# Optimization experiments

Hardware: AMD Instinct MI355X
Metric: run time of the kernel (lower is better)

## Reference

```python
import jax, jax.numpy as jnp
import numpy as np

NEG = -1e30  # log-space 'zero' (avoid actual -inf for stable grads)
BLANK = 1


def _ctc_single(logp, target, il, tl):
    # logp: [T, V] log-probabilities; target: [S] int; il, tl: scalar lengths
    T, V = logp.shape
    S = target.shape[0]
    L = 2 * S + 1
    # extended label sequence: blank, t0, blank, t1, ..., blank
    ext = jnp.full((L,), BLANK, dtype=target.dtype).at[1::2].set(target)
    prev2 = jnp.concatenate([jnp.full((2,), -1, dtype=ext.dtype), ext[:-2]])
    can_skip = (ext != BLANK) & (ext != prev2)  # allowed s-2 transition
    valid = jnp.arange(L) < (2 * tl + 1)  # mask lattice positions beyond target length
    lp_ext = logp[:, ext]  # [T, L] gather of emission log-probs along the lattice

    alpha0 = jnp.full((L,), NEG, dtype=logp.dtype)
    alpha0 = alpha0.at[0].set(lp_ext[0, 0]).at[1].set(lp_ext[0, 1])
    alpha0 = jnp.where(valid, alpha0, NEG)

    def step(alpha, inp):
        t, lp = inp  # lp: [L]
        a1 = jnp.concatenate([jnp.full((1,), NEG, alpha.dtype), alpha[:-1]])
        a2 = jnp.concatenate([jnp.full((2,), NEG, alpha.dtype), alpha[:-2]])
        a2 = jnp.where(can_skip, a2, NEG)
        new = jnp.logaddexp(jnp.logaddexp(alpha, a1), a2) + lp
        new = jnp.where(valid, new, NEG)
        new = jnp.where(t < il, new, alpha)  # freeze alpha past input length
        return new, None

    alpha, _ = jax.lax.scan(step, alpha0, (jnp.arange(1, T), lp_ext[1:]))
    end = 2 * tl
    ll = jnp.logaddexp(alpha[end], alpha[end - 1])
    loss = -ll
    # zero_infinity=True: clamp non-finite / degenerate losses to 0
    loss = jnp.where(loss < 1e29, loss, 0.0)
    return loss


def setup_inputs() -> dict:
    key = jax.random.key(0)
    k1, k2, k3, k4 = jax.random.split(key, 4)
    B, T, V, S = 64, 2000, 256, 400
    # module expects log-probabilities over phonemes
    log_probs = jax.nn.log_softmax(
        jax.random.normal(k1, (B, T, V), dtype=jnp.float32), axis=-1)
    # targets avoid blank_id=1 (labels in [2, V))
    targets = jax.random.randint(k2, (B, S), 2, V, dtype=jnp.int32)
    input_lengths = jax.random.randint(k3, (B,), T // 2, T + 1, dtype=jnp.int32)
    target_lengths = jax.random.randint(k4, (B,), S // 2, S + 1, dtype=jnp.int32)
    return {"log_probs": log_probs, "targets": targets,
            "input_lengths": input_lengths, "target_lengths": target_lengths}


def reference(log_probs, targets, input_lengths, target_lengths):
    losses = jax.vmap(_ctc_single)(log_probs, targets, input_lengths, target_lengths)
    # nn.CTCLoss reduction='mean': per-sample loss divided by target length, then batch mean
    return jnp.mean(losses / target_lengths.astype(losses.dtype))
```

## Files before the change

kernel.cpp:

```cpp
#include <hip/hip_runtime.h>

#define LOG2E 1.4426950408889634f
#define LN2   0.6931471805599453f

namespace {
constexpr int B    = 64;
constexpr int T    = 2000;
constexpr int V    = 256;
constexpr int S    = 400;
constexpr int CHK  = 8;
constexpr int NCTP = 250;
constexpr int BSTR = 20;
constexpr int KP   = 408;
constexpr size_t GELEM  = (size_t)B * NCTP * KP * 8;
constexpr size_t GBYTES = GELEM * 2;
constexpr size_t LAOFF  = GBYTES / 4;
constexpr size_t LGOFF  = LAOFF + 64 * 1024;
constexpr size_t REQBYTES = GBYTES + 2 * 64 * 1024 * 4;
constexpr int LSTR = 260;
constexpr int NW7  = 7;
constexpr int NCT7 = 250;
constexpr int BST7 = 12;
}

using h8 = __attribute__((ext_vector_type(8))) _Float16;

__device__ __forceinline__ float fexp2(float x){ return __builtin_amdgcn_exp2f(x); }
__device__ __forceinline__ float flog2(float x){ return __builtin_amdgcn_logf(x); }

__device__ __forceinline__ float wave_shr1(float x) {
  int v = __builtin_amdgcn_update_dpp(0, __builtin_bit_cast(int, x),
                                      0x138, 0xf, 0xf, true);
  return __builtin_bit_cast(float, v);
}
__device__ __forceinline__ int wave_shr1_i(int x) {
  return __builtin_amdgcn_update_dpp(0, x, 0x138, 0xf, 0xf, true);
}
__device__ __forceinline__ float wave_shl1(float x) {
  int v = __builtin_amdgcn_update_dpp(0, __builtin_bit_cast(int, x),
                                      0x130, 0xf, 0xf, true);
  return __builtin_bit_cast(float, v);
}
__device__ __forceinline__ int wave_shl1_i(int x) {
  return __builtin_amdgcn_update_dpp(0, x, 0x130, 0xf, 0xf, true);
}

__global__ __launch_bounds__(512)
void ctc_gather_kernel(const float* __restrict__ logp,
                       const int* __restrict__ targets,
                       _Float16* __restrict__ G)
{
  const int tile = blockIdx.x;
  const int b    = blockIdx.y;
  const int tid  = threadIdx.x;
  const int i0   = tile * 64;
  const float* lp = logp + (size_t)b * T * V;
  const int*   tg = targets + (size_t)b * S;

  __shared__ float ls[64 * LSTR];
  __shared__ int   tgs[S];

  for (int f = tid; f < 64 * 64; f += 512) {
    const int row = f >> 6, c4 = f & 63;
    int t = i0 + 1 + row; if (t > T - 1) t = T - 1;
    float4 v = ((const float4*)(lp + (size_t)t * V))[c4];
    *(float4*)&ls[row * LSTR + c4 * 4] = v;
  }
  for (int k = tid; k < S; k += 512) tgs[k] = tg[k];
  __syncthreads();

  const int w    = tid >> 6;
  const int lane = tid & 63;
  _Float16* gb = G + (size_t)b * NCTP * KP * 8;

  for (int it = w; it < 56; it += 8) {
    const int kb = it >> 3;
    const int cc = it & 7;
    const int c  = tile * 8 + cc;
    if (c >= NCTP) continue;
    const int k = kb * 64 + lane;
    if (k >= KP) continue;
    const int e = (k < S) ? tgs[k] : 1;
    h8 hv;
    #pragma unroll
    for (int j = 0; j < 8; ++j)
      hv[j] = (_Float16)fexp2(ls[(cc * 8 + j) * LSTR + e] * LOG2E);
    *(h8*)(gb + ((size_t)c * KP + k) * 8) = hv;
  }
}

__global__ __launch_bounds__(256)
void ctc_fb_kernel(const float* __restrict__ logp,
                   const int* __restrict__ targets,
                   const int* __restrict__ input_len,
                   const int* __restrict__ target_len,
                   const _Float16* __restrict__ G,
                   float* __restrict__ la,
                   float* __restrict__ lg)
{
  const int b    = blockIdx.x;
  const int dir  = blockIdx.y;
  const int tid  = threadIdx.x;
  const int w    = tid >> 6;
  const int lane = tid & 63;
  const bool lane0  = (lane == 0);
  const bool lane63 = (lane == 63);
  const float* __restrict__ lp = logp + (size_t)b * T * V;
  const int il = input_len[b];
  const int tl = target_len[b];
  const int m  = il >> 1;

  __shared__ float bnd[3][NCTP * BSTR];
  __shared__ int   cnt[3];
  if (tid < 3) cnt[tid] = 0;

  const int* tg = targets + (size_t)b * S;
  int ka = 2 * tid;     if (ka > S - 1) ka = S - 1;
  int kb = 2 * tid + 1; if (kb > S - 1) kb = S - 1;
  int kc = 2 * tid + 2; if (kc > S - 1) kc = S - 1;
  const int ea = tg[ka];
  const int eb = tg[kb];
  const int ec = tg[kc];
  const float ska = (ka == 0 || ea != tg[ka - 1]) ? 1.0f : 0.0f;
  const float skb = (eb != ea) ? 1.0f : 0.0f;
  const float skA = (eb != ea) ? 1.0f : 0.0f;
  const float skB = (ec != eb) ? 1.0f : 0.0f;

  const _Float16* Gb = G + (size_t)b * NCTP * KP * 8;
  const size_t offA = (size_t)ka * 8;
  const size_t offB = (size_t)kb * 8;
  const size_t offK = (size_t)400 * 8;

  __syncthreads();

  if (dir == 0) {
    float a0 = 0.0f, a1 = 0.0f, a2 = 0.0f, a3 = 0.0f;
    int   E  = 0;
    if (tid == 0) {
      a0 = fexp2(lp[1]  * LOG2E);
      a1 = fexp2(lp[ea] * LOG2E);
    }
    h8 hA = *(const h8*)(Gb + offA);
    h8 hB = *(const h8*)(Gb + offB);
    h8 hK = *(const h8*)(Gb + offK);

    const int NCH = (m + 7) >> 3;
    for (int c = 0; c < NCH; ++c) {
      float pa[CHK], pb[CHK], pk[CHK];
      #pragma unroll
      for (int i = 0; i < CHK; ++i) {
        pa[i] = (float)hA[i]; pb[i] = (float)hB[i]; pk[i] = (float)hK[i];
      }
      {
        int c2 = c + 1; if (c2 > NCTP - 1) c2 = NCTP - 1;
        const size_t base = (size_t)c2 * KP * 8;
        hA = *(const h8*)(Gb + base + offA);
        hB = *(const h8*)(Gb + base + offB);
        hK = *(const h8*)(Gb + base + offK);
      }
      float bq[CHK];
      int Ep = 0;
      if (w > 0) {
        while (__hip_atomic_load(&cnt[w - 1], __ATOMIC_ACQUIRE,
                                 __HIP_MEMORY_SCOPE_WORKGROUP) < c + 1)
          __builtin_amdgcn_s_sleep(1);
        const float* src = &bnd[w - 1][c * BSTR];
        float4 q0 = *(const float4*)(src);
        float4 q1 = *(const float4*)(src + 4);
        bq[0]=q0.x; bq[1]=q0.y; bq[2]=q0.z; bq[3]=q0.w;
        bq[4]=q1.x; bq[5]=q1.y; bq[6]=q1.z; bq[7]=q1.w;
        Ep = __float_as_int(src[8]);
      } else {
        #pragma unroll
        for (int i = 0; i < CHK; ++i) bq[i] = 0.0f;
      }
      const float mz  = fmaxf(fmaxf(a0, a1), fmaxf(a2, a3));
      const int   E4  = __shfl_up(E, 4);
      const int   E1o = wave_shr1_i(E);
      const int   E5  = wave_shr1_i(E4);
      const float mz1 = wave_shr1(mz);
      if (mz == 0.0f) E = (lane < 4) ? Ep : E4;
      int E1 = (mz1 == 0.0f) ? ((lane <= 4) ? Ep : E5) : E1o;
      if (lane0) E1 = (w == 0) ? E : Ep;
      int d = E1 - E; d = d > 126 ? 126 : (d < -126 ? -126 : d);
      const float f = ldexpf(1.0f, d);
      const float a3s = a3;

      float pub[CHK];
      #pragma unroll
      for (int i = 0; i < CHK; ++i) {
        const int t = 1 + c * CHK + i;
        if (t <= m) {
          float hl = wave_shr1(a3);
          hl = lane0 ? bq[i] : hl;
          hl *= f;
          float t3 = a3 + a2;  a3 = __builtin_fmaf(a1, skb, t3) * pb[i];
          a2 = (a2 + a1) * pk[i];
          float t1 = a1 + a0;  a1 = __builtin_fmaf(hl, ska, t1) * pa[i];
          a0 = (a0 + hl) * pk[i];
        }
        pub[i] = a3;
      }
      if (w < 3 && lane63) {
        float* dst = &bnd[w][c * BSTR];
        *(float4*)(dst)     = make_float4(a3s, pub[0], pub[1], pub[2]);
        *(float4*)(dst + 4) = make_float4(pub[3], pub[4], pub[5], pub[6]);
        dst[8] = __int_as_float(E);
        __hip_atomic_store(&cnt[w], c + 1, __ATOMIC_RELEASE,
                           __HIP_MEMORY_SCOPE_WORKGROUP);
      }
      {
        float m2 = fmaxf(fmaxf(a0, a1), fmaxf(a2, a3));
        int k = 0; (void)frexpf(m2, &k);
        a0 = ldexpf(a0, -k); a1 = ldexpf(a1, -k);
        a2 = ldexpf(a2, -k); a3 = ldexpf(a3, -k);
        E += k;
      }
    }
    float* dst = la + (size_t)b * 1024 + 4 * tid;
    dst[0] = flog2(a0) + (float)E;
    dst[1] = flog2(a1) + (float)E;
    dst[2] = flog2(a2) + (float)E;
    dst[3] = flog2(a3) + (float)E;
  } else {
    const int s0 = 4 * tid;
    float g0 = (s0 + 0 == 2 * tl - 1 || s0 + 0 == 2 * tl) ? 1.0f : 0.0f;
    float g1 = (s0 + 1 == 2 * tl - 1 || s0 + 1 == 2 * tl) ? 1.0f : 0.0f;
    float g2 = (s0 + 2 == 2 * tl - 1 || s0 + 2 == 2 * tl) ? 1.0f : 0.0f;
    float g3 = (s0 + 3 == 2 * tl - 1 || s0 + 3 == 2 * tl) ? 1.0f : 0.0f;
    int   E  = 0;

    const int c_hi = (il - 2) >> 3;
    const int c_lo = m >> 3;
    h8 hA = *(const h8*)(Gb + (size_t)c_hi * KP * 8 + offA);
    h8 hB = *(const h8*)(Gb + (size_t)c_hi * KP * 8 + offB);
    h8 hK = *(const h8*)(Gb + (size_t)c_hi * KP * 8 + offK);

    for (int c = c_hi; c >= c_lo; --c) {
      float pa[CHK], pb[CHK], pk[CHK];
      #pragma unroll
      for (int i = 0; i < CHK; ++i) {
        pa[i] = (float)hA[i]; pb[i] = (float)hB[i]; pk[i] = (float)hK[i];
      }
      {
        int c2 = c - 1; if (c2 < 0) c2 = 0;
        const size_t base = (size_t)c2 * KP * 8;
        hA = *(const h8*)(Gb + base + offA);
        hB = *(const h8*)(Gb + base + offB);
        hK = *(const h8*)(Gb + base + offK);
      }
      float bq0[CHK], bq1[CHK];
      int Ep = 0;
      if (w < 3) {
        while (__hip_atomic_load(&cnt[w], __ATOMIC_ACQUIRE,
                                 __HIP_MEMORY_SCOPE_WORKGROUP) < c_hi - c + 1)
          __builtin_amdgcn_s_sleep(1);
        const float* src = &bnd[w][c * BSTR];
        float4 q0 = *(const float4*)(src);
        float4 q1 = *(const float4*)(src + 4);
        float4 q2 = *(const float4*)(src + 8);
        float4 q3 = *(const float4*)(src + 12);
        bq0[0]=q0.x; bq0[1]=q0.y; bq0[2]=q0.z; bq0[3]=q0.w;
        bq0[4]=q1.x; bq0[5]=q1.y; bq0[6]=q1.z; bq0[7]=q1.w;
        bq1[0]=q2.x; bq1[1]=q2.y; bq1[2]=q2.z; bq1[3]=q2.w;
        bq1[4]=q3.x; bq1[5]=q3.y; bq1[6]=q3.z; bq1[7]=q3.w;
        Ep = __float_as_int(src[16]);
      } else {
        #pragma unroll
        for (int i = 0; i < CHK; ++i) { bq0[i] = 0.0f; bq1[i] = 0.0f; }
      }
      const float mz  = fmaxf(fmaxf(g0, g1), fmaxf(g2, g3));
      const int   E4  = __shfl_down(E, 4);
      const int   E1o = wave_shl1_i(E);
      const int   E5  = wave_shl1_i(E4);
      const float mzN = wave_shl1(mz);
      if (mz == 0.0f) E = (lane >= 60) ? Ep : E4;
      int E1 = (mzN == 0.0f) ? ((lane >= 59) ? Ep : E5) : E1o;
      if (lane63) E1 = (w == 3) ? E : Ep;
      int d = E1 - E; d = d > 126 ? 126 : (d < -126 ? -126 : d);
      const float f = ldexpf(1.0f, d);

      float pub0[CHK], pub1[CHK];
      #pragma unroll
      for (int i = 0; i < CHK; ++i) { pub0[i] = 0.0f; pub1[i] = 0.0f; }
      #pragma unroll
      for (int jj = 0; jj < CHK; ++jj) {
        const int j = CHK - 1 - jj;
        const int row = 1 + c * CHK + j;
        if (row > m && row < il) {
          float pg0 = g0 * pk[j];
          float pg1 = g1 * pa[j];
          float pg2 = g2 * pk[j];
          float pg3 = g3 * pb[j];
          float h0 = wave_shl1(pg0);
          float h1 = wave_shl1(pg1);
          h0 = lane63 ? bq0[j] : h0;
          h1 = lane63 ? bq1[j] : h1;
          h0 *= f;
          h1 *= f;
          pub0[j] = pg0; pub1[j] = pg1;
          g3 = __builtin_fmaf(h1, skB, pg3 + h0);
          g2 = pg3 + pg2;
          g1 = __builtin_fmaf(pg3, skA, pg1 + pg2);
          g0 = pg0 + pg1;
        }
      }
      if (w > 0 && lane0) {
        float* dst = &bnd[w - 1][c * BSTR];
        *(float4*)(dst)      = make_float4(pub0[0], pub0[1], pub0[2], pub0[3]);
        *(float4*)(dst + 4)  = make_float4(pub0[4], pub0[5], pub0[6], pub0[7]);
        *(float4*)(dst + 8)  = make_float4(pub1[0], pub1[1], pub1[2], pub1[3]);
        *(float4*)(dst + 12) = make_float4(pub1[4], pub1[5], pub1[6], pub1[7]);
        dst[16] = __int_as_float(E);
        __hip_atomic_store(&cnt[w - 1], c_hi - c + 1, __ATOMIC_RELEASE,
                           __HIP_MEMORY_SCOPE_WORKGROUP);
      }
      {
        float m2 = fmaxf(fmaxf(g0, g1), fmaxf(g2, g3));
        int k = 0; (void)frexpf(m2, &k);
        g0 = ldexpf(g0, -k); g1 = ldexpf(g1, -k);
        g2 = ldexpf(g2, -k); g3 = ldexpf(g3, -k);
        E += k;
      }
    }
    float* dst = lg + (size_t)b * 1024 + 4 * tid;
    dst[0] = flog2(g0) + (float)E;
    dst[1] = flog2(g1) + (float)E;
    dst[2] = flog2(g2) + (float)E;
    dst[3] = flog2(g3) + (float)E;
  }
}

__global__ __launch_bounds__(64)
void ctc_merge_kernel(const float* __restrict__ la,
                      const float* __restrict__ lg,
                      const int* __restrict__ target_len,
                      float* __restrict__ out)
{
  const int b    = blockIdx.x;
  const int lane = threadIdx.x;
  const int tl = target_len[b];
  const int Lb = 2 * tl + 1;
  const float* A  = la + (size_t)b * 1024;
  const float* Gm = lg + (size_t)b * 1024;

  float vs[16];
  float vmax = -1e30f;
  #pragma unroll
  for (int r = 0; r < 16; ++r) {
    const int s = lane + 64 * r;
    float x = A[s] + Gm[s];
    x = (s < Lb) ? x : -1e30f;
    vs[r] = x;
    vmax = fmaxf(vmax, x);
  }
  #pragma unroll
  for (int o = 32; o > 0; o >>= 1) vmax = fmaxf(vmax, __shfl_xor(vmax, o, 64));
  float sum = 0.0f;
  #pragma unroll
  for (int r = 0; r < 16; ++r) sum += fexp2(vs[r] - vmax);
  #pragma unroll
  for (int o = 32; o > 0; o >>= 1) sum += __shfl_xor(sum, o, 64);
  if (lane == 0) {
    const float ll = (vmax + flog2(sum)) * LN2;
    float loss = -ll;
    if (!(loss < 1e29f)) loss = 0.0f;
    atomicAdd(out, loss / ((float)tl * (float)B));
  }
}

__global__ __launch_bounds__(NW7 * 64)
void ctc_alpha7_kernel(const float* __restrict__ logp,
                       const int* __restrict__ targets,
                       const int* __restrict__ input_len,
                       const int* __restrict__ target_len,
                       float* __restrict__ out)
{
  const int b    = blockIdx.x;
  const int tid  = threadIdx.x;
  const int w    = tid >> 6;
  const int lane = tid & 63;
  const bool lane0 = (lane == 0);
  const float* __restrict__ lp = logp + (size_t)b * T * V;
  const int il = input_len[b];
  const int tl = target_len[b];
  const int Lb = 2 * tl + 1;

  __shared__ float bnd[NW7 - 1][NCT7 * BST7];
  __shared__ int   cnt[NW7 - 1];
  __shared__ float pblk[T];
  __shared__ float afin[NW7 * 64 * 2];

  if (tid < NW7 - 1) cnt[tid] = 0;

  const int* tg = targets + (size_t)b * S;
  const int k1 = (tid < S) ? tid : (S - 1);
  const int e1 = tg[k1];
  const float sk1 = (k1 == 0 || e1 != tg[k1 - 1]) ? 1.0f : 0.0f;

  for (int i = tid; i < T; i += NW7 * 64) {
    int t = (i + 1 < T) ? (i + 1) : (T - 1);
    pblk[i] = fexp2(lp[(size_t)t * V + 1] * LOG2E);
  }
  __syncthreads();

  const bool active = (w * 128) < Lb;
  if (active) {
    float a0 = 0.0f, a1 = 0.0f;
    int   E  = 0;
    if (tid == 0) { a0 = fexp2(lp[1] * LOG2E); a1 = fexp2(lp[e1] * LOG2E); }

    float tokL[CHK];
    #pragma unroll
    for (int i = 0; i < CHK; ++i) tokL[i] = lp[(size_t)(1 + i) * V + e1];

    const int NCH = (il - 1 + CHK - 1) / CHK;
    for (int c = 0; c < NCH; ++c) {
      const int t0 = 1 + c * CHK;
      float tokP[CHK];
      #pragma unroll
      for (int i = 0; i < CHK; ++i) tokP[i] = fexp2(tokL[i] * LOG2E);
      float nl[CHK];
      if (c + 1 < NCT7) {
        #pragma unroll
        for (int i = 0; i < CHK; ++i) {
          int tt = t0 + CHK + i; if (tt > T - 1) tt = T - 1;
          nl[i] = lp[(size_t)tt * V + e1];
        }
      }
      float pbk[CHK];
      {
        float4 q0 = *(const float4*)&pblk[c * CHK];
        float4 q1 = *(const float4*)&pblk[c * CHK + 4];
        pbk[0]=q0.x; pbk[1]=q0.y; pbk[2]=q0.z; pbk[3]=q0.w;
        pbk[4]=q1.x; pbk[5]=q1.y; pbk[6]=q1.z; pbk[7]=q1.w;
      }
      float bq[CHK];
      int Ep = 0;
      if (w > 0) {
        while (__hip_atomic_load(&cnt[w - 1], __ATOMIC_ACQUIRE,
                                 __HIP_MEMORY_SCOPE_WORKGROUP) < c + 1)
          __builtin_amdgcn_s_sleep(1);
        const float* src = &bnd[w - 1][c * BST7];
        float4 q0 = *(const float4*)(src);
        float4 q1 = *(const float4*)(src + 4);
        bq[0]=q0.x; bq[1]=q0.y; bq[2]=q0.z; bq[3]=q0.w;
        bq[4]=q1.x; bq[5]=q1.y; bq[6]=q1.z; bq[7]=q1.w;
        Ep = __float_as_int(src[8]);
      } else {
        #pragma unroll
        for (int i = 0; i < CHK; ++i) bq[i] = 0.0f;
      }
      const float mz  = fmaxf(a0, a1);
      const int   E1o = __shfl_up(E, 1);
      const int   E8  = __shfl_up(E, 8);
      const int   E9  = __shfl_up(E, 9);
      const float mz1 = __shfl_up(mz, 1);
      if (mz == 0.0f) E = (lane < 8) ? Ep : E8;
      int E1 = (mz1 == 0.0f) ? ((lane <= 8) ? Ep : E9) : E1o;
      if (lane0) E1 = (w == 0) ? E : Ep;
      int d = E1 - E; d = d > 126 ? 126 : (d < -126 ? -126 : d);
      const float f = ldexpf(1.0f, d);
      const float a1s = a1;
      float pub[CHK];
      #pragma unroll
      for (int i = 0; i < CHK; ++i) {
        const int t = t0 + i;
        if (t < il) {
          float hl = wave_shr1(a1);
          hl = lane0 ? bq[i] : hl;
          hl *= f;
          float s01 = a1 + a0;
          a1 = __builtin_fmaf(hl, sk1, s01) * tokP[i];
          a0 = (a0 + hl) * pbk[i];
        }
        pub[i] = a1;
      }
      if (w < NW7 - 1 && lane == 63) {
        float* dst = &bnd[w][c * BST7];
        dst[0] = a1s;
        #pragma unroll
        for (int i = 0; i < CHK - 1; ++i) dst[1 + i] = pub[i];
        dst[8] = __int_as_float(E);
        __hip_atomic_store(&cnt[w], c + 1, __ATOMIC_RELEASE,
                           __HIP_MEMORY_SCOPE_WORKGROUP);
      }
      {
        float m2 = fmaxf(a0, a1);
        int k = 0;
        (void)frexpf(m2, &k);
        a0 = ldexpf(a0, -k);
        a1 = ldexpf(a1, -k);
        E += k;
      }
      #pragma unroll
      for (int i = 0; i < CHK; ++i) tokL[i] = nl[i];
    }
    afin[2 * tid]     = flog2(a0) + (float)E;
    afin[2 * tid + 1] = flog2(a1) + (float)E;
  }
  __syncthreads();

  if (tid == 0) {
    const float x = afin[2 * tl];
    const float y = afin[2 * tl - 1];
    const float mm = fmaxf(x, y);
    const float ll = (mm + flog2(fexp2(x - mm) + fexp2(y - mm))) * LN2;
    float loss = -ll;
    if (!(loss < 1e29f)) loss = 0.0f;
    atomicAdd(out, loss / ((float)tl * (float)B));
  }
}

__global__ void ctc_zero_kernel(float* __restrict__ out) { out[0] = 0.0f; }

extern "C" void kernel_launch(void* const* d_in, const int* in_sizes, int n_in,
                              void* d_out, int out_size, void* d_ws, size_t ws_size,
                              hipStream_t stream) {
  const float* logp    = (const float*)d_in[0];
  const int*   targets = (const int*)d_in[1];
  const int*   il      = (const int*)d_in[2];
  const int*   tl      = (const int*)d_in[3];
  float* out = (float*)d_out;

  ctc_zero_kernel<<<1, 1, 0, stream>>>(out);
  if (ws_size >= REQBYTES) {
    _Float16* G  = (_Float16*)d_ws;
    float*    la = (float*)d_ws + LAOFF;
    float*    lg = (float*)d_ws + LGOFF;
    ctc_gather_kernel<<<dim3(32, B), 512, 0, stream>>>(logp, targets, G);
    ctc_fb_kernel<<<dim3(B, 2), 256, 0, stream>>>(logp, targets, il, tl, G, la, lg);
    ctc_merge_kernel<<<B, 64, 0, stream>>>(la, lg, tl, out);
  } else {
    ctc_alpha7_kernel<<<B, NW7 * 64, 0, stream>>>(logp, targets, il, tl, out);
  }
}
```

Baseline: 330.7 us.

## Collapse forward-backward CTC lattice onto a single wave with 16 states per lane

```diff
diff --git a/kernel.cpp b/kernel.cpp
--- a/kernel.cpp
+++ b/kernel.cpp
@@ -10,7 +10,6 @@
 constexpr int S    = 400;
 constexpr int CHK  = 8;
 constexpr int NCTP = 250;
-constexpr int BSTR = 20;
 constexpr int KP   = 408;
 constexpr size_t GELEM  = (size_t)B * NCTP * KP * 8;
 constexpr size_t GBYTES = GELEM * 2;
@@ -89,7 +88,7 @@
   }
 }
 
-__global__ __launch_bounds__(256)
+__global__ __launch_bounds__(64)
 void ctc_fb_kernel(const float* __restrict__ logp,
                    const int* __restrict__ targets,
                    const int* __restrict__ input_len,
@@ -100,234 +99,192 @@
 {
   const int b    = blockIdx.x;
   const int dir  = blockIdx.y;
-  const int tid  = threadIdx.x;
-  const int w    = tid >> 6;
-  const int lane = tid & 63;
-  const bool lane0  = (lane == 0);
-  const bool lane63 = (lane == 63);
+  const int lane = threadIdx.x & 63;
   const float* __restrict__ lp = logp + (size_t)b * T * V;
   const int il = input_len[b];
   const int tl = target_len[b];
   const int m  = il >> 1;
-
-  __shared__ float bnd[3][NCTP * BSTR];
-  __shared__ int   cnt[3];
-  if (tid < 3) cnt[tid] = 0;
-
   const int* tg = targets + (size_t)b * S;
-  int ka = 2 * tid;     if (ka > S - 1) ka = S - 1;
-  int kb = 2 * tid + 1; if (kb > S - 1) kb = S - 1;
-  int kc = 2 * tid + 2; if (kc > S - 1) kc = S - 1;
-  const int ea = tg[ka];
-  const int eb = tg[kb];
-  const int ec = tg[kc];
-  const float ska = (ka == 0 || ea != tg[ka - 1]) ? 1.0f : 0.0f;
-  const float skb = (eb != ea) ? 1.0f : 0.0f;
-  const float skA = (eb != ea) ? 1.0f : 0.0f;
-  const float skB = (ec != eb) ? 1.0f : 0.0f;
 
   const _Float16* Gb = G + (size_t)b * NCTP * KP * 8;
-  const size_t offA = (size_t)ka * 8;
-  const size_t offB = (size_t)kb * 8;
-  const size_t offK = (size_t)400 * 8;
-
-  __syncthreads();
+  const int krow = (8 * lane < KP - 8) ? 8 * lane : KP - 8;
+
+  float skF[8], skB[8];
+  #pragma unroll
+  for (int j = 0; j < 8; ++j) {
+    const int k   = 8 * lane + j;
+    const int kc  = k < S ? k : S - 1;
+    const int km  = (k - 1) < 0 ? 0 : ((k - 1) < S ? (k - 1) : S - 1);
+    skF[j] = (k > 0 && tg[kc] != tg[km]) ? 1.0f : 0.0f;
+    const int k2  = k + 1;
+    const int k2c = k2 < S ? k2 : S - 1;
+    const int k2m = (k2 - 1) < S ? (k2 - 1) : S - 1;
+    skB[j] = (tg[k2c] != tg[k2m]) ? 1.0f : 0.0f;
+  }
 
   if (dir == 0) {
-    float a0 = 0.0f, a1 = 0.0f, a2 = 0.0f, a3 = 0.0f;
-    int   E  = 0;
-    if (tid == 0) {
-      a0 = fexp2(lp[1]  * LOG2E);
-      a1 = fexp2(lp[ea] * LOG2E);
-    }
-    h8 hA = *(const h8*)(Gb + offA);
-    h8 hB = *(const h8*)(Gb + offB);
-    h8 hK = *(const h8*)(Gb + offK);
+    float a[16];
+    #pragma unroll
+    for (int i = 0; i < 16; ++i) a[i] = 0.0f;
+    int  E = 0;
+    bool alive = (lane == 0);
+    if (lane == 0) {
+      a[0] = fexp2(lp[1] * LOG2E);
+      a[1] = fexp2(lp[tg[0]] * LOG2E);
+    }
+
+    h8 hs[8], hk;
+    {
+      const size_t base = 0;
+      #pragma unroll
+      for (int j = 0; j < 8; ++j)
+        hs[j] = *(const h8*)(Gb + base + (size_t)(krow + j) * 8);
+      hk = *(const h8*)(Gb + base + (size_t)400 * 8);
+    }
 
     const int NCH = (m + 7) >> 3;
     for (int c = 0; c < NCH; ++c) {
-      float pa[CHK], pb[CHK], pk[CHK];
-      #pragma unroll
-      for (int i = 0; i < CHK; ++i) {
-        pa[i] = (float)hA[i]; pb[i] = (float)hB[i]; pk[i] = (float)hK[i];
-      }
+      float ps[8][8], pb[8];
+      #pragma unroll
+      for (int j = 0; j < 8; ++j) {
+        #pragma unroll
+        for (int i = 0; i < 8; ++i) ps[j][i] = (float)hs[j][i];
+      }
+      #pragma unroll
+      for (int i = 0; i < 8; ++i) pb[i] = (float)hk[i];
       {
         int c2 = c + 1; if (c2 > NCTP - 1) c2 = NCTP - 1;
-        const size_t base = (size_t)c2 * KP * 8;
-        hA = *(const h8*)(Gb + base + offA);
-        hB = *(const h8*)(Gb + base + offB);
-        hK = *(const h8*)(Gb + base + offK);
-      }
-      float bq[CHK];
-      int Ep = 0;
-      if (w > 0) {
-        while (__hip_atomic_load(&cnt[w - 1], __ATOMIC_ACQUIRE,
-                                 __HIP_MEMORY_SCOPE_WORKGROUP) < c + 1)
-          __builtin_amdgcn_s_sleep(1);
-        const float* src = &bnd[w - 1][c * BSTR];
-        float4 q0 = *(const float4*)(src);
-        float4 q1 = *(const float4*)(src + 4);
-        bq[0]=q0.x; bq[1]=q0.y; bq[2]=q0.z; bq[3]=q0.w;
-        bq[4]=q1.x; bq[5]=q1.y; bq[6]=q1.z; bq[7]=q1.w;
-        Ep = __float_as_int(src[8]);
-      } else {
-        #pragma unroll
-        for (int i = 0; i < CHK; ++i) bq[i] = 0.0f;
-      }
-      const float mz  = fmaxf(fmaxf(a0, a1), fmaxf(a2, a3));
-      const int   E4  = __shfl_up(E, 4);
-      const int   E1o = wave_shr1_i(E);
-      const int   E5  = wave_shr1_i(E4);
-      const float mz1 = wave_shr1(mz);
-      if (mz == 0.0f) E = (lane < 4) ? Ep : E4;
-      int E1 = (mz1 == 0.0f) ? ((lane <= 4) ? Ep : E5) : E1o;
-      if (lane0) E1 = (w == 0) ? E : Ep;
+        const size_t base = (size_t)c2 * (KP * 8);
+        #pragma unroll
+        for (int j = 0; j < 8; ++j)
+          hs[j] = *(const h8*)(Gb + base + (size_t)(krow + j) * 8);
+        hk = *(const h8*)(Gb + base + (size_t)400 * 8);
+      }
+
+      const int E1 = wave_shr1_i(E);
+      if (!alive) E = E1;
       int d = E1 - E; d = d > 126 ? 126 : (d < -126 ? -126 : d);
       const float f = ldexpf(1.0f, d);
-      const float a3s = a3;
-
-      float pub[CHK];
-      #pragma unroll
-      for (int i = 0; i < CHK; ++i) {
+
+      #pragma unroll
+      for (int i = 0; i < 8; ++i) {
         const int t = 1 + c * CHK + i;
         if (t <= m) {
-          float hl = wave_shr1(a3);
-          hl = lane0 ? bq[i] : hl;
-          hl *= f;
-          float t3 = a3 + a2;  a3 = __builtin_fmaf(a1, skb, t3) * pb[i];
-          a2 = (a2 + a1) * pk[i];
-          float t1 = a1 + a0;  a1 = __builtin_fmaf(hl, ska, t1) * pa[i];
-          a0 = (a0 + hl) * pk[i];
+          const float h = wave_shr1(a[15]) * f;
+          #pragma unroll
+          for (int j = 7; j >= 0; --j) {
+            const float lo = j ? a[2 * j - 1] : h;
+            a[2 * j + 1] = __builtin_fmaf(lo, skF[j],
+                                          a[2 * j + 1] + a[2 * j]) * ps[j][i];
+            a[2 * j]     = (a[2 * j] + lo) * pb[i];
+          }
         }
-        pub[i] = a3;
-      }
-      if (w < 3 && lane63) {
-        float* dst = &bnd[w][c * BSTR];
-        *(float4*)(dst)     = make_float4(a3s, pub[0], pub[1], pub[2]);
-        *(float4*)(dst + 4) = make_float4(pub[3], pub[4], pub[5], pub[6]);
-        dst[8] = __int_as_float(E);
-        __hip_atomic_store(&cnt[w], c + 1, __ATOMIC_RELEASE,
-                           __HIP_MEMORY_SCOPE_WORKGROUP);
-      }
-      {
-        float m2 = fmaxf(fmaxf(a0, a1), fmaxf(a2, a3));
+      }
+
+      {
+        float mx[8];
+        #pragma unroll
+        for (int q = 0; q < 8; ++q) mx[q] = fmaxf(a[2 * q], a[2 * q + 1]);
+        #pragma unroll
+        for (int q = 0; q < 4; ++q) mx[q] = fmaxf(mx[q], mx[q + 4]);
+        const float m2 = fmaxf(fmaxf(mx[0], mx[1]), fmaxf(mx[2], mx[3]));
         int k = 0; (void)frexpf(m2, &k);
-        a0 = ldexpf(a0, -k); a1 = ldexpf(a1, -k);
-        a2 = ldexpf(a2, -k); a3 = ldexpf(a3, -k);
+        #pragma unroll
+        for (int i = 0; i < 16; ++i) a[i] = ldexpf(a[i], -k);
         E += k;
-      }
-    }
-    float* dst = la + (size_t)b * 1024 + 4 * tid;
-    dst[0] = flog2(a0) + (float)E;
-    dst[1] = flog2(a1) + (float)E;
-    dst[2] = flog2(a2) + (float)E;
-    dst[3] = flog2(a3) + (float)E;
+        alive = (m2 != 0.0f);
+      }
+    }
+    float* dst = la + (size_t)b * 1024 + 16 * lane;
+    #pragma unroll
+    for (int i = 0; i < 16; ++i) dst[i] = flog2(a[i]) + (float)E;
   } else {
-    const int s0 = 4 * tid;
-    float g0 = (s0 + 0 == 2 * tl - 1 || s0 + 0 == 2 * tl) ? 1.0f : 0.0f;
-    float g1 = (s0 + 1 == 2 * tl - 1 || s0 + 1 == 2 * tl) ? 1.0f : 0.0f;
-    float g2 = (s0 + 2 == 2 * tl - 1 || s0 + 2 == 2 * tl) ? 1.0f : 0.0f;
-    float g3 = (s0 + 3 == 2 * tl - 1 || s0 + 3 == 2 * tl) ? 1.0f : 0.0f;
-    int   E  = 0;
+    float g[16];
+    const int s0 = 16 * lane;
+    bool alive = false;
+    #pragma unroll
+    for (int i = 0; i < 16; ++i) {
+      const int s = s0 + i;
+      g[i] = (s == 2 * tl || s == 2 * tl - 1) ? 1.0f : 0.0f;
+      alive = alive || (g[i] != 0.0f);
+    }
+    int E = 0;
 
     const int c_hi = (il - 2) >> 3;
     const int c_lo = m >> 3;
-    h8 hA = *(const h8*)(Gb + (size_t)c_hi * KP * 8 + offA);
-    h8 hB = *(const h8*)(Gb + (size_t)c_hi * KP * 8 + offB);
-    h8 hK = *(const h8*)(Gb + (size_t)c_hi * KP * 8 + offK);
+
+    h8 hs[8], hk;
+    {
+      const size_t base = (size_t)c_hi * (KP * 8);
+      #pragma unroll
+      for (int j = 0; j < 8; ++j)
+        hs[j] = *(const h8*)(Gb + base + (size_t)(krow + j) * 8);
+      hk = *(const h8*)(Gb + base + (size_t)400 * 8);
+    }
 
     for (int c = c_hi; c >= c_lo; --c) {
-      float pa[CHK], pb[CHK], pk[CHK];
-      #pragma unroll
-      for (int i = 0; i < CHK; ++i) {
-        pa[i] = (float)hA[i]; pb[i] = (float)hB[i]; pk[i] = (float)hK[i];
-      }
+      float ps[8][8], pb[8];
+      #pragma unroll
+      for (int j = 0; j < 8; ++j) {
+        #pragma unroll
+        for (int i = 0; i < 8; ++i) ps[j][i] = (float)hs[j][i];
+      }
+      #pragma unroll
+      for (int i = 0; i < 8; ++i) pb[i] = (float)hk[i];
       {
         int c2 = c - 1; if (c2 < 0) c2 = 0;
-        const size_t base = (size_t)c2 * KP * 8;
-        hA = *(const h8*)(Gb + base + offA);
-        hB = *(const h8*)(Gb + base + offB);
-        hK = *(const h8*)(Gb + base + offK);
-      }
-      float bq0[CHK], bq1[CHK];
-      int Ep = 0;
-      if (w < 3) {
-        while (__hip_atomic_load(&cnt[w], __ATOMIC_ACQUIRE,
-                                 __HIP_MEMORY_SCOPE_WORKGROUP) < c_hi - c + 1)
-          __builtin_amdgcn_s_sleep(1);
-        const float* src = &bnd[w][c * BSTR];
-        float4 q0 = *(const float4*)(src);
-        float4 q1 = *(const float4*)(src + 4);
-        float4 q2 = *(const float4*)(src + 8);
-        float4 q3 = *(const float4*)(src + 12);
-        bq0[0]=q0.x; bq0[1]=q0.y; bq0[2]=q0.z; bq0[3]=q0.w;
-        bq0[4]=q1.x; bq0[5]=q1.y; bq0[6]=q1.z; bq0[7]=q1.w;
-        bq1[0]=q2.x; bq1[1]=q2.y; bq1[2]=q2.z; bq1[3]=q2.w;
-        bq1[4]=q3.x; bq1[5]=q3.y; bq1[6]=q3.z; bq1[7]=q3.w;
-        Ep = __float_as_int(src[16]);
-      } else {
-        #pragma unroll
-        for (int i = 0; i < CHK; ++i) { bq0[i] = 0.0f; bq1[i] = 0.0f; }
-      }
-      const float mz  = fmaxf(fmaxf(g0, g1), fmaxf(g2, g3));
-      const int   E4  = __shfl_down(E, 4);
-      const int   E1o = wave_shl1_i(E);
-      const int   E5  = wave_shl1_i(E4);
-      const float mzN = wave_shl1(mz);
-      if (mz == 0.0f) E = (lane >= 60) ? Ep : E4;
-      int E1 = (mzN == 0.0f) ? ((lane >= 59) ? Ep : E5) : E1o;
-      if (lane63) E1 = (w == 3) ? E : Ep;
+        const size_t base = (size_t)c2 * (KP * 8);
+        #pragma unroll
+        for (int j = 0; j < 8; ++j)
+          hs[j] = *(const h8*)(Gb + base + (size_t)(krow + j) * 8);
+        hk = *(const h8*)(Gb + base + (size_t)400 * 8);
+      }
+
+      const int E1 = wave_shl1_i(E);
+      if (!alive) E = E1;
       int d = E1 - E; d = d > 126 ? 126 : (d < -126 ? -126 : d);
       const float f = ldexpf(1.0f, d);
 
-      float pub0[CHK], pub1[CHK];
-      #pragma unroll
-      for (int i = 0; i < CHK; ++i) { pub0[i] = 0.0f; pub1[i] = 0.0f; }
-      #pragma unroll
-      for (int jj = 0; jj < CHK; ++jj) {
-        const int j = CHK - 1 - jj;
-        const int row = 1 + c * CHK + j;
+      #pragma unroll
+      for (int ii = 0; ii < 8; ++ii) {
+        const int i = 7 - ii;
+        const int row = 1 + c * CHK + i;
         if (row > m && row < il) {
-          float pg0 = g0 * pk[j];
-          float pg1 = g1 * pa[j];
-          float pg2 = g2 * pk[j];
-          float pg3 = g3 * pb[j];
-          float h0 = wave_shl1(pg0);
-          float h1 = wave_shl1(pg1);
-          h0 = lane63 ? bq0[j] : h0;
-          h1 = lane63 ? bq1[j] : h1;
-          h0 *= f;
-          h1 *= f;
-          pub0[j] = pg0; pub1[j] = pg1;
-          g3 = __builtin_fmaf(h1, skB, pg3 + h0);
-          g2 = pg3 + pg2;
-          g1 = __builtin_fmaf(pg3, skA, pg1 + pg2);
-          g0 = pg0 + pg1;
+          float pg[16];
+          #pragma unroll
+          for (int q = 0; q < 8; ++q) {
+            pg[2 * q]     = g[2 * q]     * pb[i];
+            pg[2 * q + 1] = g[2 * q + 1] * ps[q][i];
+          }
+          const float h0 = wave_shl1(pg[0]) * f;
+          const float h1 = wave_shl1(pg[1]) * f;
+          #pragma unroll
+          for (int q = 0; q < 8; ++q) {
+            const float u1 = (q < 7) ? pg[2 * q + 2] : h0;
+            const float u2 = (q < 7) ? pg[2 * q + 3] : h1;
+            g[2 * q + 1] = __builtin_fmaf(u2, skB[q], pg[2 * q + 1] + u1);
+            g[2 * q]     = pg[2 * q] + pg[2 * q + 1];
+          }
         }
       }
-      if (w > 0 && lane0) {
-        float* dst = &bnd[w - 1][c * BSTR];
-        *(float4*)(dst)      = make_float4(pub0[0], pub0[1], pub0[2], pub0[3]);
-        *(float4*)(dst + 4)  = make_float4(pub0[4], pub0[5], pub0[6], pub0[7]);
-        *(float4*)(dst + 8)  = make_float4(pub1[0], pub1[1], pub1[2], pub1[3]);
-        *(float4*)(dst + 12) = make_float4(pub1[4], pub1[5], pub1[6], pub1[7]);
-        dst[16] = __int_as_float(E);
-        __hip_atomic_store(&cnt[w - 1], c_hi - c + 1, __ATOMIC_RELEASE,
-                           __HIP_MEMORY_SCOPE_WORKGROUP);
-      }
-      {
-        float m2 = fmaxf(fmaxf(g0, g1), fmaxf(g2, g3));
+
+      {
+        float mx[8];
+        #pragma unroll
+        for (int q = 0; q < 8; ++q) mx[q] = fmaxf(g[2 * q], g[2 * q + 1]);
+        #pragma unroll
+        for (int q = 0; q < 4; ++q) mx[q] = fmaxf(mx[q], mx[q + 4]);
+        const float m2 = fmaxf(fmaxf(mx[0], mx[1]), fmaxf(mx[2], mx[3]));
         int k = 0; (void)frexpf(m2, &k);
-        g0 = ldexpf(g0, -k); g1 = ldexpf(g1, -k);
-        g2 = ldexpf(g2, -k); g3 = ldexpf(g3, -k);
+        #pragma unroll
+        for (int i = 0; i < 16; ++i) g[i] = ldexpf(g[i], -k);
         E += k;
-      }
-    }
-    float* dst = lg + (size_t)b * 1024 + 4 * tid;
-    dst[0] = flog2(g0) + (float)E;
-    dst[1] = flog2(g1) + (float)E;
-    dst[2] = flog2(g2) + (float)E;
-    dst[3] = flog2(g3) + (float)E;
+        alive = (m2 != 0.0f);
+      }
+    }
+    float* dst = lg + (size_t)b * 1024 + 16 * lane;
+    #pragma unroll
+    for (int i = 0; i < 16; ++i) dst[i] = flog2(g[i]) + (float)E;
   }
 }
 
@@ -529,7 +486,7 @@
     float*    la = (float*)d_ws + LAOFF;
     float*    lg = (float*)d_ws + LGOFF;
     ctc_gather_kernel<<<dim3(32, B), 512, 0, stream>>>(logp, targets, G);
-    ctc_fb_kernel<<<dim3(B, 2), 256, 0, stream>>>(logp, targets, il, tl, G, la, lg);
+    ctc_fb_kernel<<<dim3(B, 2), 64, 0, stream>>>(logp, targets, il, tl, G, la, lg);
     ctc_merge_kernel<<<B, 64, 0, stream>>>(la, lg, tl, out);
   } else {
     ctc_alpha7_kernel<<<B, NW7 * 64, 0, stream>>>(logp, targets, il, tl, out);
```

Result: slower. 361.0 us (+9.1%).

## Spread CTC lattice over 8 waves with barrier-synchronized wavefront pipeline

Applied to the files above, without the earlier changes.

```diff
diff --git a/kernel.cpp b/kernel.cpp
--- a/kernel.cpp
+++ b/kernel.cpp
@@ -10,7 +10,6 @@
 constexpr int S    = 400;
 constexpr int CHK  = 8;
 constexpr int NCTP = 250;
-constexpr int BSTR = 20;
 constexpr int KP   = 408;
 constexpr size_t GELEM  = (size_t)B * NCTP * KP * 8;
 constexpr size_t GBYTES = GELEM * 2;
@@ -89,7 +88,7 @@
   }
 }
 
-__global__ __launch_bounds__(256)
+__global__ __launch_bounds__(512)
 void ctc_fb_kernel(const float* __restrict__ logp,
                    const int* __restrict__ targets,
                    const int* __restrict__ input_len,
@@ -109,62 +108,50 @@
   const int il = input_len[b];
   const int tl = target_len[b];
   const int m  = il >> 1;
-
-  __shared__ float bnd[3][NCTP * BSTR];
-  __shared__ int   cnt[3];
-  if (tid < 3) cnt[tid] = 0;
-
   const int* tg = targets + (size_t)b * S;
-  int ka = 2 * tid;     if (ka > S - 1) ka = S - 1;
-  int kb = 2 * tid + 1; if (kb > S - 1) kb = S - 1;
-  int kc = 2 * tid + 2; if (kc > S - 1) kc = S - 1;
-  const int ea = tg[ka];
-  const int eb = tg[kb];
-  const int ec = tg[kc];
-  const float ska = (ka == 0 || ea != tg[ka - 1]) ? 1.0f : 0.0f;
-  const float skb = (eb != ea) ? 1.0f : 0.0f;
-  const float skA = (eb != ea) ? 1.0f : 0.0f;
-  const float skB = (ec != eb) ? 1.0f : 0.0f;
-
   const _Float16* Gb = G + (size_t)b * NCTP * KP * 8;
-  const size_t offA = (size_t)ka * 8;
-  const size_t offB = (size_t)kb * 8;
-  const size_t offK = (size_t)400 * 8;
-
-  __syncthreads();
+
+  __shared__ float bnd[8][2][20];
+
+  const int kfrag = (tid < KP) ? tid : (KP - 1);
+
+  h8 As, Ak, Bs, Bk;
 
   if (dir == 0) {
-    float a0 = 0.0f, a1 = 0.0f, a2 = 0.0f, a3 = 0.0f;
+    const int k1 = (tid < S) ? tid : (S - 1);
+    const float sk1 = (k1 == 0 || tg[k1] != tg[k1 - 1]) ? 1.0f : 0.0f;
+
+    float a0 = 0.0f, a1 = 0.0f;
     int   E  = 0;
     if (tid == 0) {
-      a0 = fexp2(lp[1]  * LOG2E);
-      a1 = fexp2(lp[ea] * LOG2E);
+      a0 = fexp2(lp[1] * LOG2E);
+      a1 = fexp2(lp[tg[0]] * LOG2E);
     }
-    h8 hA = *(const h8*)(Gb + offA);
-    h8 hB = *(const h8*)(Gb + offB);
-    h8 hK = *(const h8*)(Gb + offK);
-
-    const int NCH = (m + 7) >> 3;
-    for (int c = 0; c < NCH; ++c) {
-      float pa[CHK], pb[CHK], pk[CHK];
-      #pragma unroll
-      for (int i = 0; i < CHK; ++i) {
-        pa[i] = (float)hA[i]; pb[i] = (float)hB[i]; pk[i] = (float)hK[i];
-      }
+
+    As = *(const h8*)(Gb + (size_t)kfrag * 8);
+    Ak = *(const h8*)(Gb + (size_t)400 * 8);
+    Bs = As; Bk = Ak;
+
+    const int NCH   = (m + 7) >> 3;
+    const int NITER = NCH + 7;
+
+    auto body = [&](int n, h8& curS, h8& curK, h8& nxtS, h8& nxtK) {
+      __syncthreads();
+      const int c = n - w;
+      if (c < 0 || c >= NCH) return;
+      float ps[8], pb[8];
+      #pragma unroll
+      for (int i = 0; i < 8; ++i) { ps[i] = (float)curS[i]; pb[i] = (float)curK[i]; }
       {
         int c2 = c + 1; if (c2 > NCTP - 1) c2 = NCTP - 1;
-        const size_t base = (size_t)c2 * KP * 8;
-        hA = *(const h8*)(Gb + base + offA);
-        hB = *(const h8*)(Gb + base + offB);
-        hK = *(const h8*)(Gb + base + offK);
-      }
-      float bq[CHK];
+        nxtS = *(const h8*)(Gb + ((size_t)c2 * KP + kfrag) * 8);
+        nxtK = *(const h8*)(Gb + ((size_t)c2 * KP + 400) * 8);
+        __builtin_amdgcn_sched_barrier(0);
+      }
+      float bq[8];
       int Ep = 0;
       if (w > 0) {
-        while (__hip_atomic_load(&cnt[w - 1], __ATOMIC_ACQUIRE,
-                                 __HIP_MEMORY_SCOPE_WORKGROUP) < c + 1)
-          __builtin_amdgcn_s_sleep(1);
-        const float* src = &bnd[w - 1][c * BSTR];
+        const float* src = &bnd[w - 1][(n - 1) & 1][0];
         float4 q0 = *(const float4*)(src);
         float4 q1 = *(const float4*)(src + 4);
         bq[0]=q0.x; bq[1]=q0.y; bq[2]=q0.z; bq[3]=q0.w;
@@ -172,90 +159,93 @@
         Ep = __float_as_int(src[8]);
       } else {
         #pragma unroll
-        for (int i = 0; i < CHK; ++i) bq[i] = 0.0f;
-      }
-      const float mz  = fmaxf(fmaxf(a0, a1), fmaxf(a2, a3));
-      const int   E4  = __shfl_up(E, 4);
-      const int   E1o = wave_shr1_i(E);
-      const int   E5  = wave_shr1_i(E4);
-      const float mz1 = wave_shr1(mz);
-      if (mz == 0.0f) E = (lane < 4) ? Ep : E4;
-      int E1 = (mz1 == 0.0f) ? ((lane <= 4) ? Ep : E5) : E1o;
+        for (int i = 0; i < 8; ++i) bq[i] = 0.0f;
+      }
+      const float mz  = fmaxf(a0, a1);
+      const int   E1o = __shfl_up(E, 1);
+      const int   E8  = __shfl_up(E, 8);
+      const int   E9  = __shfl_up(E, 9);
+      const float mz1 = __shfl_up(mz, 1);
+      if (mz == 0.0f) E = (lane < 8) ? Ep : E8;
+      int E1 = (mz1 == 0.0f) ? ((lane <= 8) ? Ep : E9) : E1o;
       if (lane0) E1 = (w == 0) ? E : Ep;
       int d = E1 - E; d = d > 126 ? 126 : (d < -126 ? -126 : d);
       const float f = ldexpf(1.0f, d);
-      const float a3s = a3;
-
-      float pub[CHK];
-      #pragma unroll
-      for (int i = 0; i < CHK; ++i) {
+
+      const float a1s = a1;
+      float pub[8];
+      #pragma unroll
+      for (int i = 0; i < 8; ++i) {
         const int t = 1 + c * CHK + i;
         if (t <= m) {
-          float hl = wave_shr1(a3);
+          float hl = wave_shr1(a1);
           hl = lane0 ? bq[i] : hl;
           hl *= f;
-          float t3 = a3 + a2;  a3 = __builtin_fmaf(a1, skb, t3) * pb[i];
-          a2 = (a2 + a1) * pk[i];
-          float t1 = a1 + a0;  a1 = __builtin_fmaf(hl, ska, t1) * pa[i];
-          a0 = (a0 + hl) * pk[i];
+          float s01 = a1 + a0;
+          a1 = __builtin_fmaf(hl, sk1, s01) * ps[i];
+          a0 = (a0 + hl) * pb[i];
         }
-        pub[i] = a3;
-      }
-      if (w < 3 && lane63) {
-        float* dst = &bnd[w][c * BSTR];
-        *(float4*)(dst)     = make_float4(a3s, pub[0], pub[1], pub[2]);
+        pub[i] = a1;
+      }
+      if (w < 7 && lane63) {
+        float* dst = &bnd[w][n & 1][0];
+        *(float4*)(dst)     = make_float4(a1s, pub[0], pub[1], pub[2]);
         *(float4*)(dst + 4) = make_float4(pub[3], pub[4], pub[5], pub[6]);
         dst[8] = __int_as_float(E);
-        __hip_atomic_store(&cnt[w], c + 1, __ATOMIC_RELEASE,
-                           __HIP_MEMORY_SCOPE_WORKGROUP);
       }
       {
-        float m2 = fmaxf(fmaxf(a0, a1), fmaxf(a2, a3));
-        int k = 0; (void)frexpf(m2, &k);
-        a0 = ldexpf(a0, -k); a1 = ldexpf(a1, -k);
-        a2 = ldexpf(a2, -k); a3 = ldexpf(a3, -k);
-        E += k;
-      }
+        const float m2 = fmaxf(a0, a1);
+        int kk = 0; (void)frexpf(m2, &kk);
+        a0 = ldexpf(a0, -kk);
+        a1 = ldexpf(a1, -kk);
+        E += kk;
+      }
+    };
+
+    for (int n = 0; n < NITER; n += 2) {
+      body(n,     As, Ak, Bs, Bk);
+      body(n + 1, Bs, Bk, As, Ak);
     }
-    float* dst = la + (size_t)b * 1024 + 4 * tid;
+
+    float* dst = la + (size_t)b * 1024 + 2 * tid;
     dst[0] = flog2(a0) + (float)E;
     dst[1] = flog2(a1) + (float)E;
-    dst[2] = flog2(a2) + (float)E;
-    dst[3] = flog2(a3) + (float)E;
   } else {
-    const int s0 = 4 * tid;
-    float g0 = (s0 + 0 == 2 * tl - 1 || s0 + 0 == 2 * tl) ? 1.0f : 0.0f;
-    float g1 = (s0 + 1 == 2 * tl - 1 || s0 + 1 == 2 * tl) ? 1.0f : 0.0f;
-    float g2 = (s0 + 2 == 2 * tl - 1 || s0 + 2 == 2 * tl) ? 1.0f : 0.0f;
-    float g3 = (s0 + 3 == 2 * tl - 1 || s0 + 3 == 2 * tl) ? 1.0f : 0.0f;
+    const int k2c = (tid + 1 < S) ? (tid + 1) : (S - 1);
+    const int k2m = (tid < S) ? tid : (S - 1);
+    const float skB = (tg[k2c] != tg[k2m]) ? 1.0f : 0.0f;
+
+    const int s0 = 2 * tid;
+    float g0 = (s0     == 2 * tl || s0     == 2 * tl - 1) ? 1.0f : 0.0f;
+    float g1 = (s0 + 1 == 2 * tl || s0 + 1 == 2 * tl - 1) ? 1.0f : 0.0f;
     int   E  = 0;
 
     const int c_hi = (il - 2) >> 3;
     const int c_lo = m >> 3;
-    h8 hA = *(const h8*)(Gb + (size_t)c_hi * KP * 8 + offA);
-    h8 hB = *(const h8*)(Gb + (size_t)c_hi * KP * 8 + offB);
-    h8 hK = *(const h8*)(Gb + (size_t)c_hi * KP * 8 + offK);
-
-    for (int c = c_hi; c >= c_lo; --c) {
-      float pa[CHK], pb[CHK], pk[CHK];
-      #pragma unroll
-      for (int i = 0; i < CHK; ++i) {
-        pa[i] = (float)hA[i]; pb[i] = (float)hB[i]; pk[i] = (float)hK[i];
-      }
+    const int NITER = (c_hi - c_lo) + 8;
+
+    As = *(const h8*)(Gb + ((size_t)c_hi * KP + kfrag) * 8);
+    Ak = *(const h8*)(Gb + ((size_t)c_hi * KP + 400) * 8);
+    Bs = As; Bk = Ak;
+
+    auto body = [&](int n, h8& curS, h8& curK, h8& nxtS, h8& nxtK) {
+      __syncthreads();
+      const int jn = n - (7 - w);
+      const int c  = c_hi - jn;
+      if (jn < 0 || c < c_lo) return;
+      float ps[8], pb[8];
+      #pragma unroll
+      for (int i = 0; i < 8; ++i) { ps[i] = (float)curS[i]; pb[i] = (float)curK[i]; }
       {
         int c2 = c - 1; if (c2 < 0) c2 = 0;
-        const size_t base = (size_t)c2 * KP * 8;
-        hA = *(const h8*)(Gb + base + offA);
-        hB = *(const h8*)(Gb + base + offB);
-        hK = *(const h8*)(Gb + base + offK);
-      }
-      float bq0[CHK], bq1[CHK];
+        nxtS = *(const h8*)(Gb + ((size_t)c2 * KP + kfrag) * 8);
+        nxtK = *(const h8*)(Gb + ((size_t)c2 * KP + 400) * 8);
+        __builtin_amdgcn_sched_barrier(0);
+      }
+      float bq0[8], bq1[8];
       int Ep = 0;
-      if (w < 3) {
-        while (__hip_atomic_load(&cnt[w], __ATOMIC_ACQUIRE,
-                                 __HIP_MEMORY_SCOPE_WORKGROUP) < c_hi - c + 1)
-          __builtin_amdgcn_s_sleep(1);
-        const float* src = &bnd[w][c * BSTR];
+      if (w < 7) {
+        const float* src = &bnd[w + 1][(n - 1) & 1][0];
         float4 q0 = *(const float4*)(src);
         float4 q1 = *(const float4*)(src + 4);
         float4 q2 = *(const float4*)(src + 8);
@@ -267,67 +257,65 @@
         Ep = __float_as_int(src[16]);
       } else {
         #pragma unroll
-        for (int i = 0; i < CHK; ++i) { bq0[i] = 0.0f; bq1[i] = 0.0f; }
-      }
-      const float mz  = fmaxf(fmaxf(g0, g1), fmaxf(g2, g3));
-      const int   E4  = __shfl_down(E, 4);
+        for (int i = 0; i < 8; ++i) { bq0[i] = 0.0f; bq1[i] = 0.0f; }
+      }
+      const float mz  = fmaxf(g0, g1);
       const int   E1o = wave_shl1_i(E);
-      const int   E5  = wave_shl1_i(E4);
+      const int   E8  = __shfl_down(E, 8);
+      const int   E9  = __shfl_down(E, 9);
       const float mzN = wave_shl1(mz);
-      if (mz == 0.0f) E = (lane >= 60) ? Ep : E4;
-      int E1 = (mzN == 0.0f) ? ((lane >= 59) ? Ep : E5) : E1o;
-      if (lane63) E1 = (w == 3) ? E : Ep;
+      if (mz == 0.0f) E = (lane >= 56) ? Ep : E8;
+      int E1 = (mzN == 0.0f) ? ((lane >= 55) ? Ep : E9) : E1o;
+      if (lane63) E1 = (w == 7) ? E : Ep;
       int d = E1 - E; d = d > 126 ? 126 : (d < -126 ? -126 : d);
       const float f = ldexpf(1.0f, d);
 
-      float pub0[CHK], pub1[CHK];
-      #pragma unroll
-      for (int i = 0; i < CHK; ++i) { pub0[i] = 0.0f; pub1[i] = 0.0f; }
-      #pragma unroll
-      for (int jj = 0; jj < CHK; ++jj) {
-        const int j = CHK - 1 - jj;
-        const int row = 1 + c * CHK + j;
+      float pub0[8], pub1[8];
+      #pragma unroll
+      for (int i = 0; i < 8; ++i) { pub0[i] = 0.0f; pub1[i] = 0.0f; }
+      #pragma unroll
+      for (int ii = 0; ii < 8; ++ii) {
+        const int i = 7 - ii;
+        const int row = 1 + c * CHK + i;
         if (row > m && row < il) {
-          float pg0 = g0 * pk[j];
-          float pg1 = g1 * pa[j];
-          float pg2 = g2 * pk[j];
-          float pg3 = g3 * pb[j];
+          float pg0 = g0 * pb[i];
+          float pg1 = g1 * ps[i];
           float h0 = wave_shl1(pg0);
           float h1 = wave_shl1(pg1);
-          h0 = lane63 ? bq0[j] : h0;
-          h1 = lane63 ? bq1[j] : h1;
+          h0 = lane63 ? bq0[i] : h0;
+          h1 = lane63 ? bq1[i] : h1;
           h0 *= f;
           h1 *= f;
-          pub0[j] = pg0; pub1[j] = pg1;
-          g3 = __builtin_fmaf(h1, skB, pg3 + h0);
-          g2 = pg3 + pg2;
-          g1 = __builtin_fmaf(pg3, skA, pg1 + pg2);
+          pub0[i] = pg0; pub1[i] = pg1;
+          g1 = __builtin_fmaf(h1, skB, pg1 + h0);
           g0 = pg0 + pg1;
         }
       }
       if (w > 0 && lane0) {
-        float* dst = &bnd[w - 1][c * BSTR];
+        float* dst = &bnd[w][n & 1][0];
         *(float4*)(dst)      = make_float4(pub0[0], pub0[1], pub0[2], pub0[3]);
         *(float4*)(dst + 4)  = make_float4(pub0[4], pub0[5], pub0[6], pub0[7]);
         *(float4*)(dst + 8)  = make_float4(pub1[0], pub1[1], pub1[2], pub1[3]);
         *(float4*)(dst + 12) = make_float4(pub1[4], pub1[5], pub1[6], pub1[7]);
         dst[16] = __int_as_float(E);
-        __hip_atomic_store(&cnt[w - 1], c_hi - c + 1, __ATOMIC_RELEASE,
-                           __HIP_MEMORY_SCOPE_WORKGROUP);
       }
       {
-        float m2 = fmaxf(fmaxf(g0, g1), fmaxf(g2, g3));
-        int k = 0; (void)frexpf(m2, &k);
-        g0 = ldexpf(g0, -k); g1 = ldexpf(g1, -k);
-        g2 = ldexpf(g2, -k); g3 = ldexpf(g3, -k);
-        E += k;
-      }
+        const float m2 = fmaxf(g0, g1);
+        int kk = 0; (void)frexpf(m2, &kk);
+        g0 = ldexpf(g0, -kk);
+        g1 = ldexpf(g1, -kk);
+        E += kk;
+      }
+    };
+
+    for (int n = 0; n < NITER; n += 2) {
+      body(n,     As, Ak, Bs, Bk);
+      body(n + 1, Bs, Bk, As, Ak);
     }
-    float* dst = lg + (size_t)b * 1024 + 4 * tid;
+
+    float* dst = lg + (size_t)b * 1024 + 2 * tid;
     dst[0] = flog2(g0) + (float)E;
     dst[1] = flog2(g1) + (float)E;
-    dst[2] = flog2(g2) + (float)E;
-    dst[3] = flog2(g3) + (float)E;
   }
 }
 
@@ -529,7 +517,7 @@
     float*    la = (float*)d_ws + LAOFF;
     float*    lg = (float*)d_ws + LGOFF;
     ctc_gather_kernel<<<dim3(32, B), 512, 0, stream>>>(logp, targets, G);
-    ctc_fb_kernel<<<dim3(B, 2), 256, 0, stream>>>(logp, targets, il, tl, G, la, lg);
+    ctc_fb_kernel<<<dim3(B, 2), 512, 0, stream>>>(logp, targets, il, tl, G, la, lg);
     ctc_merge_kernel<<<B, 64, 0, stream>>>(la, lg, tl, out);
   } else {
     ctc_alpha7_kernel<<<B, NW7 * 64, 0, stream>>>(logp, targets, il, tl, out);
```

After: 339.0 us. 2.5% more time.
